# Optimization experiments

Measured on AMD Instinct MI355X. Metric: run time of the kernel, lower is better.

The kernel has to match this reference:

```python
import jax, jax.numpy as jnp
import numpy as np
from jax import lax

D_MODEL = 1024
BATCH = 4
SEQ = 4096
DECAY = 0.9
INPUT_SCALE = 0.1


def setup_inputs() -> dict:
    key = jax.random.key(0)
    k1, k2, k3 = jax.random.split(key, 3)
    scale_in = 1.0 / np.sqrt(D_MODEL)
    return {
        "x": jax.random.normal(k1, (BATCH, SEQ, D_MODEL), dtype=jnp.float32),
        "W_in": jax.random.normal(k2, (D_MODEL, 2 * D_MODEL), dtype=jnp.float32) * scale_in,
        "b_in": jnp.zeros((2 * D_MODEL,), dtype=jnp.float32),
        "W_out": jax.random.normal(k3, (D_MODEL, D_MODEL), dtype=jnp.float32) * scale_in,
        "b_out": jnp.zeros((D_MODEL,), dtype=jnp.float32),
    }


def reference(x, W_in, b_in, W_out, b_out):
    # x: [B, S, D]
    x_proj = jnp.einsum("bsd,de->bse", x, W_in) + b_in  # [B, S, 2D]
    x_gate, x_hidden = jnp.split(x_proj, 2, axis=-1)
    x_gated = jax.nn.sigmoid(x_gate) * jax.nn.silu(x_hidden)  # [B, S, D]

    # gated EMA scan: h_t = 0.9*h_{t-1} + 0.1*g_t, h_0 = 0
    def step(h, g_t):
        h = DECAY * h + INPUT_SCALE * g_t
        return h, h

    g_tm = jnp.swapaxes(x_gated, 0, 1)  # [S, B, D] time-major
    h0 = jnp.zeros((x.shape[0], x.shape[2]), dtype=x.dtype)
    _, hs = lax.scan(step, h0, g_tm)  # [S, B, D]
    hidden_seq = jnp.swapaxes(hs, 0, 1)  # [B, S, D]

    out = jnp.einsum("bsd,de->bse", hidden_seq, W_out) + b_out
    return out
```

## Files before the change

kernel.cpp:

```cpp
#include <hip/hip_runtime.h>
#include <hip/hip_bf16.h>

#define B_   4
#define S_   4096
#define D_   1024
#define M_   (B_ * S_)
#define K_   1024
#define BK   64
#define NT   (K_ / BK)

typedef __attribute__((ext_vector_type(4))) float f32x4;
typedef __attribute__((ext_vector_type(8))) short bf16x8;
typedef unsigned short ushort_t;
typedef unsigned int uint_t;

#define SCHEDB __builtin_amdgcn_sched_barrier(0)
#define MFMA16(a, b, c) __builtin_amdgcn_mfma_f32_16x16x32_bf16(a, b, c, 0, 0, 0)

__device__ inline ushort_t f2bf(float f) {
    union { float f; unsigned u; } v; v.f = f;
    unsigned r = v.u + 0x7fffu + ((v.u >> 16) & 1u);
    return (ushort_t)(r >> 16);
}
__device__ inline float bf2f(ushort_t s) {
    union { unsigned u; float f; } v; v.u = ((unsigned)s) << 16; return v.f;
}

__global__ void convert_x_kernel(const float4* __restrict__ x, ushort_t* __restrict__ xb) {
    int i = blockIdx.x * 256 + threadIdx.x;
    float4 a = x[2 * i], b = x[2 * i + 1];
    union { ushort_t s[8]; uint4 v; } u;
    u.s[0] = f2bf(a.x); u.s[1] = f2bf(a.y); u.s[2] = f2bf(a.z); u.s[3] = f2bf(a.w);
    u.s[4] = f2bf(b.x); u.s[5] = f2bf(b.y); u.s[6] = f2bf(b.z); u.s[7] = f2bf(b.w);
    ((uint4*)xb)[i] = u.v;
}

__global__ void transpose_win_kernel(const float* __restrict__ W, ushort_t* __restrict__ WT) {
    __shared__ float tile[32][33];
    int tx = threadIdx.x, ty = threadIdx.y;
    int n0 = blockIdx.x * 32, k0 = blockIdx.y * 32;
    int ci = (n0 >> 1) + (tx & 15) + ((tx & 16) ? 1024 : 0);
    tile[ty][tx] = W[(long)(k0 + ty) * 2048 + ci];
    __syncthreads();
    WT[(long)(n0 + ty) * 1024 + k0 + tx] = f2bf(tile[tx][ty]);
}

__global__ void transpose_wo_kernel(const float* __restrict__ W, ushort_t* __restrict__ WT) {
    __shared__ float tile[32][33];
    int tx = threadIdx.x, ty = threadIdx.y;
    int n0 = blockIdx.x * 32, k0 = blockIdx.y * 32;
    tile[ty][tx] = W[(long)(k0 + ty) * 1024 + n0 + tx];
    __syncthreads();
    WT[(long)(n0 + ty) * 1024 + k0 + tx] = f2bf(tile[tx][ty]);
}

__device__ inline void stage_half(const char* gtile, char* ldst, int soff0, int soff1, int w) {
    __builtin_amdgcn_global_load_lds((const __attribute__((address_space(1))) void*)(gtile + soff0),
                                     (__attribute__((address_space(3))) void*)(ldst + w * 2048), 16, 0, 0);
    __builtin_amdgcn_global_load_lds((const __attribute__((address_space(1))) void*)(gtile + soff1),
                                     (__attribute__((address_space(3))) void*)(ldst + w * 2048 + 1024), 16, 0, 0);
}

template<int NBN, int GATE>
__global__ __launch_bounds__(512, 2) void gemm8_kernel(
    const ushort_t* __restrict__ A, const ushort_t* __restrict__ Bm,
    const float* __restrict__ bias, void* __restrict__ outp)
{
    extern __shared__ char smem[];
    const int tid = threadIdx.x;
    const int l = tid & 63, w = tid >> 6;
    const int wm = w >> 2, wn = w & 3;
    const int lrow = l & 15, kgrp = l >> 4;

    const int nwg = gridDim.x;
    const int cpx = nwg >> 3;
    const int bid = blockIdx.x;
    const int wg = (bid & 7) * cpx + (bid >> 3);
    const long m0 = (long)(wg / NBN) * 256;
    const long n0 = (long)(wg % NBN) * 256;

    const char* gA = (const char*)A + m0 * 2048;
    const char* gB = (const char*)Bm + n0 * 2048;

    const int lsw = (((l & 7) ^ (l >> 3)) << 4);
    const int soff0 = ((w * 2 + 0) * 8 + (l >> 3)) * 2048 + lsw;
    const int soff1 = ((w * 2 + 1) * 8 + (l >> 3)) * 2048 + lsw;

    const int arow = (wm * 128 + lrow) * 128;
    const int brow = (wn * 64 + lrow) * 128;
    const int sw0 = (((0 * 4 + kgrp) ^ (l & 7)) << 4);
    const int sw1 = (((1 * 4 + kgrp) ^ (l & 7)) << 4);

    f32x4 acc[8][4];
#pragma unroll
    for (int i = 0; i < 8; ++i)
#pragma unroll
        for (int j = 0; j < 4; ++j) acc[i][j] = f32x4{0.f, 0.f, 0.f, 0.f};

#define STAGE_TILE(t, buf)                                                    \
    do {                                                                      \
        const char* sa_ = gA + (t) * 128;                                     \
        const char* sb_ = gB + (t) * 128;                                     \
        stage_half(sa_,          (buf),          soff0, soff1, w);            \
        stage_half(sa_ + 262144, (buf) + 16384,  soff0, soff1, w);            \
        stage_half(sb_,          (buf) + 32768,  soff0, soff1, w);            \
        stage_half(sb_ + 262144, (buf) + 49152,  soff0, soff1, w);            \
    } while (0)

    STAGE_TILE(0, smem);
    STAGE_TILE(1, smem + 65536);
    asm volatile("s_waitcnt vmcnt(8)" ::: "memory");
    __builtin_amdgcn_s_barrier();
    SCHEDB;

    bf16x8 a0[8], b0[4], a1[8], b1[4];
#pragma unroll
    for (int fm = 0; fm < 8; ++fm) a0[fm] = *(const bf16x8*)(smem + arow + fm * 2048 + sw0);
#pragma unroll
    for (int fn = 0; fn < 4; ++fn) b0[fn] = *(const bf16x8*)(smem + 32768 + brow + fn * 2048 + sw0);

    for (int t = 0; t < NT; ++t) {
        char* cA = smem + ((t & 1) << 16);
        char* cB = cA + 32768;
        char* nA = smem + (((t + 1) & 1) << 16);
        char* nB = nA + 32768;

#pragma unroll
        for (int fm = 0; fm < 8; ++fm) a1[fm] = *(const bf16x8*)(cA + arow + fm * 2048 + sw1);
#pragma unroll
        for (int fn = 0; fn < 4; ++fn) b1[fn] = *(const bf16x8*)(cB + brow + fn * 2048 + sw1);

        asm volatile("s_waitcnt lgkmcnt(12)" ::: "memory");
        SCHEDB;

        __builtin_amdgcn_s_setprio(1);
#pragma unroll
        for (int fm = 0; fm < 8; ++fm)
#pragma unroll
            for (int fn = 0; fn < 4; ++fn)
                acc[fm][fn] = MFMA16(a0[fm], b0[fn], acc[fm][fn]);
        __builtin_amdgcn_s_setprio(0);
        SCHEDB;

        asm volatile("s_waitcnt lgkmcnt(0)" ::: "memory");
        asm volatile("s_waitcnt vmcnt(0)" ::: "memory");
        __builtin_amdgcn_s_barrier();
        SCHEDB;

        if (t + 2 < NT) STAGE_TILE(t + 2, cA);

        if (t + 1 < NT) {
#pragma unroll
            for (int fm = 0; fm < 8; ++fm) a0[fm] = *(const bf16x8*)(nA + arow + fm * 2048 + sw0);
#pragma unroll
            for (int fn = 0; fn < 4; ++fn) b0[fn] = *(const bf16x8*)(nB + brow + fn * 2048 + sw0);
        }
        SCHEDB;

        __builtin_amdgcn_s_setprio(1);
#pragma unroll
        for (int fm = 0; fm < 8; ++fm)
#pragma unroll
            for (int fn = 0; fn < 4; ++fn)
                acc[fm][fn] = MFMA16(a1[fm], b1[fn], acc[fm][fn]);
        __builtin_amdgcn_s_setprio(0);
        SCHEDB;
    }
#undef STAGE_TILE

    const long row0 = m0 + wm * 128 + kgrp * 4;
    if (GATE) {
        ushort_t* g = (ushort_t*)outp;
#pragma unroll
        for (int fm = 0; fm < 8; ++fm) {
#pragma unroll
            for (int fp = 0; fp < 2; ++fp) {
                int c = (int)(n0 >> 1) + wn * 32 + fp * 16 + lrow;
                float bg = bias[c], bh = bias[1024 + c];
#pragma unroll
                for (int r = 0; r < 4; ++r) {
                    long rr = row0 + fm * 16 + r;
                    float gate = acc[fm][fp * 2][r] + bg;
                    float hid  = acc[fm][fp * 2 + 1][r] + bh;
                    float sg = 1.0f / (1.0f + expf(-gate));
                    float sh = 1.0f / (1.0f + expf(-hid));
                    g[rr * 1024 + c] = f2bf(sg * hid * sh);
                }
            }
        }
    } else {
        float* o = (float*)outp;
#pragma unroll
        for (int fm = 0; fm < 8; ++fm)
#pragma unroll
            for (int fn = 0; fn < 4; ++fn) {
                int c = (int)n0 + wn * 64 + fn * 16 + lrow;
                float bo = bias[c];
#pragma unroll
                for (int r = 0; r < 4; ++r) {
                    long rr = row0 + fm * 16 + r;
                    o[rr * 1024 + c] = acc[fm][fn][r] + bo;
                }
            }
    }
}

__global__ void scan_kernel(const ushort_t* __restrict__ g, ushort_t* __restrict__ h) {
    int idx = blockIdx.x * 256 + threadIdx.x;
    int b = idx >> 9, d = (idx & 511) * 2;
    int chunk = blockIdx.y;
    const ushort_t* gb = g + (long)b * S_ * 1024 + d;
    ushort_t* hb = h + (long)b * S_ * 1024 + d;
    float h0 = 0.f, h1 = 0.f;
    int t0 = chunk * 256;
    int tw = t0 - 96; if (tw < 0) tw = 0;
    for (int t = tw; t < t0; ++t) {
        uint_t v = *(const uint_t*)(gb + (long)t * 1024);
        h0 = 0.9f * h0 + 0.1f * bf2f((ushort_t)(v & 0xffffu));
        h1 = 0.9f * h1 + 0.1f * bf2f((ushort_t)(v >> 16));
    }
    for (int t = t0; t < t0 + 256; ++t) {
        uint_t v = *(const uint_t*)(gb + (long)t * 1024);
        h0 = 0.9f * h0 + 0.1f * bf2f((ushort_t)(v & 0xffffu));
        h1 = 0.9f * h1 + 0.1f * bf2f((ushort_t)(v >> 16));
        *(uint_t*)(hb + (long)t * 1024) = (((uint_t)f2bf(h1)) << 16) | (uint_t)f2bf(h0);
    }
}

extern "C" void kernel_launch(void* const* d_in, const int* in_sizes, int n_in,
                              void* d_out, int out_size, void* d_ws, size_t ws_size,
                              hipStream_t stream) {
    const float* x     = (const float*)d_in[0];
    const float* W_in  = (const float*)d_in[1];
    const float* b_in  = (const float*)d_in[2];
    const float* W_out = (const float*)d_in[3];
    const float* b_out = (const float*)d_in[4];
    float* outp = (float*)d_out;

    char* ws = (char*)d_ws;
    ushort_t* xb   = (ushort_t*)ws;
    ushort_t* winT = (ushort_t*)(ws + 33554432);
    ushort_t* woT  = (ushort_t*)(ws + 33554432 + 4194304);
    ushort_t* gbuf = (ushort_t*)(ws + 33554432 + 6291456);

    hipFuncSetAttribute((const void*)&gemm8_kernel<8, 1>, hipFuncAttributeMaxDynamicSharedMemorySize, 131072);
    hipFuncSetAttribute((const void*)&gemm8_kernel<4, 0>, hipFuncAttributeMaxDynamicSharedMemorySize, 131072);

    convert_x_kernel<<<8192, 256, 0, stream>>>((const float4*)x, xb);
    transpose_win_kernel<<<dim3(64, 32), dim3(32, 32), 0, stream>>>(W_in, winT);
    transpose_wo_kernel<<<dim3(32, 32), dim3(32, 32), 0, stream>>>(W_out, woT);
    gemm8_kernel<8, 1><<<512, 512, 131072, stream>>>(xb, winT, b_in, (void*)gbuf);
    scan_kernel<<<dim3(8, 16), 256, 0, stream>>>(gbuf, xb);
    gemm8_kernel<4, 0><<<256, 512, 131072, stream>>>(xb, woT, b_out, (void*)outp);
}
```

Measured before the change: 205.7 us.

## Switch GEMM main loop to 4-stage BK=32 LDS pipeline with prefetch depth 3

Halves the K-tile to 32 and replaces the double-buffered BK=64 loop with a four-buffer ring, issuing global-to-LDS loads three tiles ahead with graduated vmcnt waits. The LDS layout and XOR swizzle are redone for 64-byte rows. The aim is to hide global-load latency better by keeping more loads in flight. In exchange there are twice as many barriers per K, and the register-level double buffering of A/B fragments is dropped, so LDS reads now wait fully before the MFMAs.

```diff
diff --git a/kernel.cpp b/kernel.cpp
--- a/kernel.cpp
+++ b/kernel.cpp
@@ -6,7 +6,7 @@
 #define D_   1024
 #define M_   (B_ * S_)
 #define K_   1024
-#define BK   64
+#define BK   32
 #define NT   (K_ / BK)
 
 typedef __attribute__((ext_vector_type(4))) float f32x4;
@@ -54,11 +54,17 @@
     WT[(long)(n0 + ty) * 1024 + k0 + tx] = f2bf(tile[tx][ty]);
 }
 
-__device__ inline void stage_half(const char* gtile, char* ldst, int soff0, int soff1, int w) {
-    __builtin_amdgcn_global_load_lds((const __attribute__((address_space(1))) void*)(gtile + soff0),
-                                     (__attribute__((address_space(3))) void*)(ldst + w * 2048), 16, 0, 0);
-    __builtin_amdgcn_global_load_lds((const __attribute__((address_space(1))) void*)(gtile + soff1),
-                                     (__attribute__((address_space(3))) void*)(ldst + w * 2048 + 1024), 16, 0, 0);
+__device__ inline void stage4(const char* ga, const char* gb, char* buf,
+                              int so0, int so1, int w) {
+    int ld = w * 2048;
+    __builtin_amdgcn_global_load_lds((const __attribute__((address_space(1))) void*)(ga + so0),
+                                     (__attribute__((address_space(3))) void*)(buf + ld), 16, 0, 0);
+    __builtin_amdgcn_global_load_lds((const __attribute__((address_space(1))) void*)(ga + so1),
+                                     (__attribute__((address_space(3))) void*)(buf + ld + 1024), 16, 0, 0);
+    __builtin_amdgcn_global_load_lds((const __attribute__((address_space(1))) void*)(gb + so0),
+                                     (__attribute__((address_space(3))) void*)(buf + 16384 + ld), 16, 0, 0);
+    __builtin_amdgcn_global_load_lds((const __attribute__((address_space(1))) void*)(gb + so1),
+                                     (__attribute__((address_space(3))) void*)(buf + 16384 + ld + 1024), 16, 0, 0);
 }
 
 template<int NBN, int GATE>
@@ -82,14 +88,17 @@
     const char* gA = (const char*)A + m0 * 2048;
     const char* gB = (const char*)Bm + n0 * 2048;
 
-    const int lsw = (((l & 7) ^ (l >> 3)) << 4);
-    const int soff0 = ((w * 2 + 0) * 8 + (l >> 3)) * 2048 + lsw;
-    const int soff1 = ((w * 2 + 1) * 8 + (l >> 3)) * 2048 + lsw;
-
-    const int arow = (wm * 128 + lrow) * 128;
-    const int brow = (wn * 64 + lrow) * 128;
-    const int sw0 = (((0 * 4 + kgrp) ^ (l & 7)) << 4);
-    const int sw1 = (((1 * 4 + kgrp) ^ (l & 7)) << 4);
+    const int r0 = (w * 2 + 0) * 16 + (l >> 2);
+    const int r1 = (w * 2 + 1) * 16 + (l >> 2);
+    const int soff0 = r0 * 2048 + ((((l & 3) - r0) & 3) << 4);
+    const int soff1 = r1 * 2048 + ((((l & 3) - r1) & 3) << 4);
+
+    const int fsw = (((kgrp + lrow) & 3) << 4);
+    int a_off[8], b_off[4];
+#pragma unroll
+    for (int fm = 0; fm < 8; ++fm) a_off[fm] = (wm * 128 + fm * 16 + lrow) * 64 + fsw;
+#pragma unroll
+    for (int fn = 0; fn < 4; ++fn) b_off[fn] = 16384 + (wn * 64 + fn * 16 + lrow) * 64 + fsw;
 
     f32x4 acc[8][4];
 #pragma unroll
@@ -97,76 +106,46 @@
 #pragma unroll
         for (int j = 0; j < 4; ++j) acc[i][j] = f32x4{0.f, 0.f, 0.f, 0.f};
 
-#define STAGE_TILE(t, buf)                                                    \
-    do {                                                                      \
-        const char* sa_ = gA + (t) * 128;                                     \
-        const char* sb_ = gB + (t) * 128;                                     \
-        stage_half(sa_,          (buf),          soff0, soff1, w);            \
-        stage_half(sa_ + 262144, (buf) + 16384,  soff0, soff1, w);            \
-        stage_half(sb_,          (buf) + 32768,  soff0, soff1, w);            \
-        stage_half(sb_ + 262144, (buf) + 49152,  soff0, soff1, w);            \
-    } while (0)
-
-    STAGE_TILE(0, smem);
-    STAGE_TILE(1, smem + 65536);
+    stage4(gA, gB, smem, soff0, soff1, w);
+    stage4(gA + 64, gB + 64, smem + 32768, soff0, soff1, w);
+    stage4(gA + 128, gB + 128, smem + 65536, soff0, soff1, w);
     asm volatile("s_waitcnt vmcnt(8)" ::: "memory");
     __builtin_amdgcn_s_barrier();
-    SCHEDB;
-
-    bf16x8 a0[8], b0[4], a1[8], b1[4];
-#pragma unroll
-    for (int fm = 0; fm < 8; ++fm) a0[fm] = *(const bf16x8*)(smem + arow + fm * 2048 + sw0);
-#pragma unroll
-    for (int fn = 0; fn < 4; ++fn) b0[fn] = *(const bf16x8*)(smem + 32768 + brow + fn * 2048 + sw0);
-
-    for (int t = 0; t < NT; ++t) {
-        char* cA = smem + ((t & 1) << 16);
-        char* cB = cA + 32768;
-        char* nA = smem + (((t + 1) & 1) << 16);
-        char* nB = nA + 32768;
-
-#pragma unroll
-        for (int fm = 0; fm < 8; ++fm) a1[fm] = *(const bf16x8*)(cA + arow + fm * 2048 + sw1);
-#pragma unroll
-        for (int fn = 0; fn < 4; ++fn) b1[fn] = *(const bf16x8*)(cB + brow + fn * 2048 + sw1);
-
-        asm volatile("s_waitcnt lgkmcnt(12)" ::: "memory");
-        SCHEDB;
-
-        __builtin_amdgcn_s_setprio(1);
-#pragma unroll
-        for (int fm = 0; fm < 8; ++fm)
-#pragma unroll
-            for (int fn = 0; fn < 4; ++fn)
-                acc[fm][fn] = MFMA16(a0[fm], b0[fn], acc[fm][fn]);
-        __builtin_amdgcn_s_setprio(0);
-        SCHEDB;
-
-        asm volatile("s_waitcnt lgkmcnt(0)" ::: "memory");
-        asm volatile("s_waitcnt vmcnt(0)" ::: "memory");
-        __builtin_amdgcn_s_barrier();
-        SCHEDB;
-
-        if (t + 2 < NT) STAGE_TILE(t + 2, cA);
-
-        if (t + 1 < NT) {
-#pragma unroll
-            for (int fm = 0; fm < 8; ++fm) a0[fm] = *(const bf16x8*)(nA + arow + fm * 2048 + sw0);
-#pragma unroll
-            for (int fn = 0; fn < 4; ++fn) b0[fn] = *(const bf16x8*)(nB + brow + fn * 2048 + sw0);
+
+    for (int tb = 0; tb < NT / 4; ++tb) {
+#pragma unroll
+        for (int q = 0; q < 4; ++q) {
+            const int t = tb * 4 + q;
+            char* cbuf = smem + (q << 15);
+            char* sbuf = smem + (((q + 3) & 3) << 15);
+
+            if (t + 3 < NT) stage4(gA + (t + 3) * 64, gB + (t + 3) * 64, sbuf, soff0, soff1, w);
+
+            bf16x8 af[8], bf[4];
+#pragma unroll
+            for (int fm = 0; fm < 8; ++fm) af[fm] = *(const bf16x8*)(cbuf + a_off[fm]);
+#pragma unroll
+            for (int fn = 0; fn < 4; ++fn) bf[fn] = *(const bf16x8*)(cbuf + b_off[fn]);
+
+            asm volatile("s_waitcnt lgkmcnt(0)" ::: "memory");
+            SCHEDB;
+            __builtin_amdgcn_s_setprio(1);
+#pragma unroll
+            for (int fm = 0; fm < 8; ++fm)
+#pragma unroll
+                for (int fn = 0; fn < 4; ++fn)
+                    acc[fm][fn] = MFMA16(af[fm], bf[fn], acc[fm][fn]);
+            __builtin_amdgcn_s_setprio(0);
+            SCHEDB;
+
+            if (t < NT - 1) {
+                if (t <= NT - 4)      asm volatile("s_waitcnt vmcnt(8)" ::: "memory");
+                else if (t == NT - 3) asm volatile("s_waitcnt vmcnt(4)" ::: "memory");
+                else                  asm volatile("s_waitcnt vmcnt(0)" ::: "memory");
+                __builtin_amdgcn_s_barrier();
+            }
         }
-        SCHEDB;
-
-        __builtin_amdgcn_s_setprio(1);
-#pragma unroll
-        for (int fm = 0; fm < 8; ++fm)
-#pragma unroll
-            for (int fn = 0; fn < 4; ++fn)
-                acc[fm][fn] = MFMA16(a1[fm], b1[fn], acc[fm][fn]);
-        __builtin_amdgcn_s_setprio(0);
-        SCHEDB;
-    }
-#undef STAGE_TILE
+    }
 
     const long row0 = m0 + wm * 128 + kgrp * 4;
     if (GATE) {
```

Result: slower. 214.8 us (+4.4%).

## Use 4-wave workgroups with 128x128 warp tiles and finer scan chunks

Applied to the files above, without the earlier changes.

The GEMM moves from 8 waves per workgroup (each computing 128x64) to 4 waves each computing a 128x128 sub-tile. This raises MFMA work per LDS fragment read and halves the number of waves sharing the same 256x256 block tile. Staging is reorganised so each wave issues 16 direct-to-LDS loads per K tile. The scan uses 128-step chunks with twice as many blocks and unrolled loops to expose more parallelism, which increases the fraction of redundant warm-up steps. The cost is doubled accumulator and fragment registers per thread (64 accumulators) and fewer waves per CU to hide latency.

```diff
diff --git a/kernel.cpp b/kernel.cpp
--- a/kernel.cpp
+++ b/kernel.cpp
@@ -54,27 +54,23 @@
     WT[(long)(n0 + ty) * 1024 + k0 + tx] = f2bf(tile[tx][ty]);
 }
 
-__device__ inline void stage_half(const char* gtile, char* ldst, int soff0, int soff1, int w) {
-    __builtin_amdgcn_global_load_lds((const __attribute__((address_space(1))) void*)(gtile + soff0),
-                                     (__attribute__((address_space(3))) void*)(ldst + w * 2048), 16, 0, 0);
-    __builtin_amdgcn_global_load_lds((const __attribute__((address_space(1))) void*)(gtile + soff1),
-                                     (__attribute__((address_space(3))) void*)(ldst + w * 2048 + 1024), 16, 0, 0);
+__device__ inline void gld16(const char* g, char* l) {
+    __builtin_amdgcn_global_load_lds((const __attribute__((address_space(1))) void*)g,
+                                     (__attribute__((address_space(3))) void*)l, 16, 0, 0);
 }
 
 template<int NBN, int GATE>
-__global__ __launch_bounds__(512, 2) void gemm8_kernel(
+__global__ __launch_bounds__(256, 1) void gemmw_kernel(
     const ushort_t* __restrict__ A, const ushort_t* __restrict__ Bm,
     const float* __restrict__ bias, void* __restrict__ outp)
 {
     extern __shared__ char smem[];
     const int tid = threadIdx.x;
     const int l = tid & 63, w = tid >> 6;
-    const int wm = w >> 2, wn = w & 3;
+    const int wm = w >> 1, wn = w & 1;
     const int lrow = l & 15, kgrp = l >> 4;
 
-    const int nwg = gridDim.x;
-    const int cpx = nwg >> 3;
-    const int bid = blockIdx.x;
+    const int nwg = gridDim.x, cpx = nwg >> 3, bid = blockIdx.x;
     const int wg = (bid & 7) * cpx + (bid >> 3);
     const long m0 = (long)(wg / NBN) * 256;
     const long n0 = (long)(wg % NBN) * 256;
@@ -83,77 +79,75 @@
     const char* gB = (const char*)Bm + n0 * 2048;
 
     const int lsw = (((l & 7) ^ (l >> 3)) << 4);
-    const int soff0 = ((w * 2 + 0) * 8 + (l >> 3)) * 2048 + lsw;
-    const int soff1 = ((w * 2 + 1) * 8 + (l >> 3)) * 2048 + lsw;
-
+    const int srow = w * 64 + (l >> 3);
     const int arow = (wm * 128 + lrow) * 128;
-    const int brow = (wn * 64 + lrow) * 128;
-    const int sw0 = (((0 * 4 + kgrp) ^ (l & 7)) << 4);
-    const int sw1 = (((1 * 4 + kgrp) ^ (l & 7)) << 4);
-
-    f32x4 acc[8][4];
+    const int brow = 32768 + (wn * 128 + lrow) * 128;
+    const int sw0 = ((kgrp ^ (l & 7)) << 4);
+    const int sw1 = (((4 + kgrp) ^ (l & 7)) << 4);
+
+    f32x4 acc[8][8];
 #pragma unroll
     for (int i = 0; i < 8; ++i)
 #pragma unroll
-        for (int j = 0; j < 4; ++j) acc[i][j] = f32x4{0.f, 0.f, 0.f, 0.f};
-
-#define STAGE_TILE(t, buf)                                                    \
-    do {                                                                      \
-        const char* sa_ = gA + (t) * 128;                                     \
-        const char* sb_ = gB + (t) * 128;                                     \
-        stage_half(sa_,          (buf),          soff0, soff1, w);            \
-        stage_half(sa_ + 262144, (buf) + 16384,  soff0, soff1, w);            \
-        stage_half(sb_,          (buf) + 32768,  soff0, soff1, w);            \
-        stage_half(sb_ + 262144, (buf) + 49152,  soff0, soff1, w);            \
+        for (int j = 0; j < 8; ++j) acc[i][j] = f32x4{0.f, 0.f, 0.f, 0.f};
+
+#define STAGEW(t, buf)                                                          \
+    do {                                                                        \
+        _Pragma("unroll")                                                       \
+        for (int j = 0; j < 8; ++j)                                             \
+            gld16(gA + (t) * 128 + (srow + j * 8) * 2048 + lsw,                 \
+                  (buf) + w * 8192 + j * 1024);                                 \
+        _Pragma("unroll")                                                       \
+        for (int j = 0; j < 8; ++j)                                             \
+            gld16(gB + (t) * 128 + (srow + j * 8) * 2048 + lsw,                 \
+                  (buf) + 32768 + w * 8192 + j * 1024);                         \
     } while (0)
 
-    STAGE_TILE(0, smem);
-    STAGE_TILE(1, smem + 65536);
-    asm volatile("s_waitcnt vmcnt(8)" ::: "memory");
+    STAGEW(0, smem);
+    STAGEW(1, smem + 65536);
+    asm volatile("s_waitcnt vmcnt(16)" ::: "memory");
     __builtin_amdgcn_s_barrier();
+
+    bf16x8 a0[8], b0[8], a1[8], b1[8];
+#pragma unroll
+    for (int fm = 0; fm < 8; ++fm) a0[fm] = *(const bf16x8*)(smem + arow + fm * 2048 + sw0);
+#pragma unroll
+    for (int fn = 0; fn < 8; ++fn) b0[fn] = *(const bf16x8*)(smem + brow + fn * 2048 + sw0);
     SCHEDB;
 
-    bf16x8 a0[8], b0[4], a1[8], b1[4];
-#pragma unroll
-    for (int fm = 0; fm < 8; ++fm) a0[fm] = *(const bf16x8*)(smem + arow + fm * 2048 + sw0);
-#pragma unroll
-    for (int fn = 0; fn < 4; ++fn) b0[fn] = *(const bf16x8*)(smem + 32768 + brow + fn * 2048 + sw0);
-
     for (int t = 0; t < NT; ++t) {
-        char* cA = smem + ((t & 1) << 16);
-        char* cB = cA + 32768;
-        char* nA = smem + (((t + 1) & 1) << 16);
-        char* nB = nA + 32768;
-
-#pragma unroll
-        for (int fm = 0; fm < 8; ++fm) a1[fm] = *(const bf16x8*)(cA + arow + fm * 2048 + sw1);
-#pragma unroll
-        for (int fn = 0; fn < 4; ++fn) b1[fn] = *(const bf16x8*)(cB + brow + fn * 2048 + sw1);
-
-        asm volatile("s_waitcnt lgkmcnt(12)" ::: "memory");
+        char* cur = smem + ((t & 1) << 16);
+        char* nxt = smem + (((t + 1) & 1) << 16);
+
+#pragma unroll
+        for (int fm = 0; fm < 8; ++fm) a1[fm] = *(const bf16x8*)(cur + arow + fm * 2048 + sw1);
+#pragma unroll
+        for (int fn = 0; fn < 8; ++fn) b1[fn] = *(const bf16x8*)(cur + brow + fn * 2048 + sw1);
+
+        asm volatile("s_waitcnt lgkmcnt(15)" ::: "memory");
         SCHEDB;
 
         __builtin_amdgcn_s_setprio(1);
 #pragma unroll
         for (int fm = 0; fm < 8; ++fm)
 #pragma unroll
-            for (int fn = 0; fn < 4; ++fn)
+            for (int fn = 0; fn < 8; ++fn)
                 acc[fm][fn] = MFMA16(a0[fm], b0[fn], acc[fm][fn]);
         __builtin_amdgcn_s_setprio(0);
         SCHEDB;
 
         asm volatile("s_waitcnt lgkmcnt(0)" ::: "memory");
         asm volatile("s_waitcnt vmcnt(0)" ::: "memory");
-        __builtin_amdgcn_s_barrier();
-        SCHEDB;
-
-        if (t + 2 < NT) STAGE_TILE(t + 2, cA);
+        if (t < NT - 1) __builtin_amdgcn_s_barrier();
+        SCHEDB;
+
+        if (t + 2 < NT) STAGEW(t + 2, cur);
 
         if (t + 1 < NT) {
 #pragma unroll
-            for (int fm = 0; fm < 8; ++fm) a0[fm] = *(const bf16x8*)(nA + arow + fm * 2048 + sw0);
-#pragma unroll
-            for (int fn = 0; fn < 4; ++fn) b0[fn] = *(const bf16x8*)(nB + brow + fn * 2048 + sw0);
+            for (int fm = 0; fm < 8; ++fm) a0[fm] = *(const bf16x8*)(nxt + arow + fm * 2048 + sw0);
+#pragma unroll
+            for (int fn = 0; fn < 8; ++fn) b0[fn] = *(const bf16x8*)(nxt + brow + fn * 2048 + sw0);
         }
         SCHEDB;
 
@@ -161,12 +155,12 @@
 #pragma unroll
         for (int fm = 0; fm < 8; ++fm)
 #pragma unroll
-            for (int fn = 0; fn < 4; ++fn)
+            for (int fn = 0; fn < 8; ++fn)
                 acc[fm][fn] = MFMA16(a1[fm], b1[fn], acc[fm][fn]);
         __builtin_amdgcn_s_setprio(0);
         SCHEDB;
     }
-#undef STAGE_TILE
+#undef STAGEW
 
     const long row0 = m0 + wm * 128 + kgrp * 4;
     if (GATE) {
@@ -174,8 +168,8 @@
 #pragma unroll
         for (int fm = 0; fm < 8; ++fm) {
 #pragma unroll
-            for (int fp = 0; fp < 2; ++fp) {
-                int c = (int)(n0 >> 1) + wn * 32 + fp * 16 + lrow;
+            for (int fp = 0; fp < 4; ++fp) {
+                int c = (int)(n0 >> 1) + wn * 64 + fp * 16 + lrow;
                 float bg = bias[c], bh = bias[1024 + c];
 #pragma unroll
                 for (int r = 0; r < 4; ++r) {
@@ -193,8 +187,8 @@
 #pragma unroll
         for (int fm = 0; fm < 8; ++fm)
 #pragma unroll
-            for (int fn = 0; fn < 4; ++fn) {
-                int c = (int)n0 + wn * 64 + fn * 16 + lrow;
+            for (int fn = 0; fn < 8; ++fn) {
+                int c = (int)n0 + wn * 128 + fn * 16 + lrow;
                 float bo = bias[c];
 #pragma unroll
                 for (int r = 0; r < 4; ++r) {
@@ -212,14 +206,16 @@
     const ushort_t* gb = g + (long)b * S_ * 1024 + d;
     ushort_t* hb = h + (long)b * S_ * 1024 + d;
     float h0 = 0.f, h1 = 0.f;
-    int t0 = chunk * 256;
+    int t0 = chunk * 128;
     int tw = t0 - 96; if (tw < 0) tw = 0;
+#pragma unroll 4
     for (int t = tw; t < t0; ++t) {
         uint_t v = *(const uint_t*)(gb + (long)t * 1024);
         h0 = 0.9f * h0 + 0.1f * bf2f((ushort_t)(v & 0xffffu));
         h1 = 0.9f * h1 + 0.1f * bf2f((ushort_t)(v >> 16));
     }
-    for (int t = t0; t < t0 + 256; ++t) {
+#pragma unroll 4
+    for (int t = t0; t < t0 + 128; ++t) {
         uint_t v = *(const uint_t*)(gb + (long)t * 1024);
         h0 = 0.9f * h0 + 0.1f * bf2f((ushort_t)(v & 0xffffu));
         h1 = 0.9f * h1 + 0.1f * bf2f((ushort_t)(v >> 16));
@@ -243,13 +239,13 @@
     ushort_t* woT  = (ushort_t*)(ws + 33554432 + 4194304);
     ushort_t* gbuf = (ushort_t*)(ws + 33554432 + 6291456);
 
-    hipFuncSetAttribute((const void*)&gemm8_kernel<8, 1>, hipFuncAttributeMaxDynamicSharedMemorySize, 131072);
-    hipFuncSetAttribute((const void*)&gemm8_kernel<4, 0>, hipFuncAttributeMaxDynamicSharedMemorySize, 131072);
+    hipFuncSetAttribute((const void*)&gemmw_kernel<8, 1>, hipFuncAttributeMaxDynamicSharedMemorySize, 131072);
+    hipFuncSetAttribute((const void*)&gemmw_kernel<4, 0>, hipFuncAttributeMaxDynamicSharedMemorySize, 131072);
 
     convert_x_kernel<<<8192, 256, 0, stream>>>((const float4*)x, xb);
     transpose_win_kernel<<<dim3(64, 32), dim3(32, 32), 0, stream>>>(W_in, winT);
     transpose_wo_kernel<<<dim3(32, 32), dim3(32, 32), 0, stream>>>(W_out, woT);
-    gemm8_kernel<8, 1><<<512, 512, 131072, stream>>>(xb, winT, b_in, (void*)gbuf);
-    scan_kernel<<<dim3(8, 16), 256, 0, stream>>>(gbuf, xb);
-    gemm8_kernel<4, 0><<<256, 512, 131072, stream>>>(xb, woT, b_out, (void*)outp);
-}
+    gemmw_kernel<8, 1><<<512, 256, 131072, stream>>>(xb, winT, b_in, (void*)gbuf);
+    scan_kernel<<<dim3(8, 32), 256, 0, stream>>>(gbuf, xb);
+    gemmw_kernel<4, 0><<<256, 256, 131072, stream>>>(xb, woT, b_out, (void*)outp);
+}
```

New measurement: 191.1 us. 7.1% less time.
